# Optimization experiments

Hardware: AMD Instinct MI355X
Metric: run time of the kernel (lower is better)

Reference implementation:

```python
import jax, jax.numpy as jnp
import numpy as np

B, S, H = 32, 128, 768
MH, MT = 6, 8            # max holder / target span sizes
M = max(MH, MT)          # max span size -> M conv widths (1..M)
KH, KT = 4, 4            # max n holders / targets per sentence


def _forward(embedding, mask, wh, bh, wt, bt, wi, bi, we, be):
    Bz, Sz, Hz = embedding.shape
    # --- multi-scale span averaging (Conv1d with identity box filters == moving mean) ---
    cs = jnp.concatenate([jnp.zeros((Bz, 1, Hz), embedding.dtype),
                          jnp.cumsum(embedding, axis=1)], axis=1)  # [B,S+1,H]
    reps = [embedding]
    for w in range(2, M + 1):
        mean = (cs[:, w:, :] - cs[:, :-w, :]) / float(w)          # [B,S-w+1,H]
        reps.append(jnp.pad(mean, ((0, 0), (0, w - 1), (0, 0))))  # zero-pad tail like torch.cat
    span = jnp.concatenate(reps, axis=1)                          # [B, M*S, H]; index = S*width_idx + start
    # --- span validity masks (span must fit within sentence length) ---
    lengths = jnp.sum(mask, axis=1)                               # [B]
    pos = jnp.arange(Sz)
    widths = jnp.arange(M)
    base = pos[None, None, :] < (lengths[:, None, None] - widths[None, :, None])  # [B,M,S]
    holder_valid = (base & (widths[None, :, None] < MH)).reshape(Bz, M * Sz)
    target_valid = (base & (widths[None, :, None] < MT)).reshape(Bz, M * Sz)
    # --- span scoring (sigmoid linear), invalid spans forced to -1 ---
    hs = jnp.where(holder_valid, jax.nn.sigmoid(span @ wh + bh), -1.0)  # [B, M*S]
    ts = jnp.where(target_valid, jax.nn.sigmoid(span @ wt + bt), -1.0)
    # --- top-k span selection (== argsort descending, take first K) ---
    vt, it = jax.lax.top_k(ts, KT)
    vh, ih = jax.lax.top_k(hs, KH)
    tval = vt > 0.0                                                # [B,KT]
    hval = vh > 0.0                                                # [B,KH]
    trep = jnp.take_along_axis(span, it[:, :, None], axis=1)      # [B,KT,H]
    hrep = jnp.take_along_axis(span, ih[:, :, None], axis=1)      # [B,KH,H]
    implicit_input = trep * tval[:, :, None].astype(span.dtype)   # zeros where invalid
    pair_valid = (hval[:, :, None] & tval[:, None, :])            # [B,KH,KT]
    pair = jnp.concatenate([jnp.broadcast_to(hrep[:, :, None, :], (Bz, KH, KT, Hz)),
                            jnp.broadcast_to(trep[:, None, :, :], (Bz, KH, KT, Hz))], axis=-1)
    explicit_input = (pair * pair_valid[..., None].astype(span.dtype)).reshape(Bz, KH * KT, 2 * Hz)
    implicit_logits = implicit_input @ wi + bi                    # [B,KT,4]
    explicit_logits = explicit_input @ we + be                    # [B,KH*KT,4]
    return implicit_logits, explicit_logits, hs, ts


def setup_inputs() -> dict:
    key = jax.random.key(0)
    ks = jax.random.split(key, 8)
    embedding = jax.random.normal(ks[0], (B, S, H), jnp.float32)
    mask = jax.random.randint(ks[1], (B, S), 0, 2).astype(jnp.int32)
    wh = jax.random.normal(ks[2], (H,), jnp.float32) * 0.02
    bh = jnp.zeros((), jnp.float32)
    wt = jax.random.normal(ks[3], (H,), jnp.float32) * 0.02
    bt = jnp.zeros((), jnp.float32)
    wi = jax.random.normal(ks[4], (H, 4), jnp.float32) * 0.02
    bi = jnp.zeros((4,), jnp.float32)
    we = jax.random.normal(ks[5], (2 * H, 4), jnp.float32) * 0.02
    be = jnp.zeros((4,), jnp.float32)
    return dict(embedding=embedding, mask=mask, wh=wh, bh=bh, wt=wt, bt=bt,
                wi=wi, bi=bi, we=we, be=be)


def reference(embedding, mask, wh, bh, wt, bt, wi, bi, we, be):
    return _forward(embedding, mask, wh, bh, wt, bt, wi, bi, we, be)
```

## Files before the change

### kernel.cpp

```cpp
#include <hip/hip_runtime.h>

namespace {
constexpr int Bsz = 32;
constexpr int Ssz = 128;
constexpr int Hsz = 768;
constexpr int Msz = 8;
constexpr int MHs = 6;
constexpr int NSPAN = Msz * Ssz;
}

__device__ __forceinline__ bool gtpair(float av, int ai, float bv, int bi) {
    return (av > bv) || (av == bv && ai < bi);
}

struct Top4 { float v[4]; int ix[4]; };

__device__ __forceinline__ void t4_init(Top4& t) {
#pragma unroll
    for (int k = 0; k < 4; ++k) { t.v[k] = -3.f; t.ix[k] = 0x7fffffff; }
}

__device__ __forceinline__ void t4_insert_g(Top4& a, float cv, int ci) {
    bool g0 = gtpair(cv, ci, a.v[0], a.ix[0]);
    bool g1 = gtpair(cv, ci, a.v[1], a.ix[1]);
    bool g2 = gtpair(cv, ci, a.v[2], a.ix[2]);
    bool g3 = gtpair(cv, ci, a.v[3], a.ix[3]);
    float nv3 = g2 ? a.v[2]  : (g3 ? cv : a.v[3]);
    int   ni3 = g2 ? a.ix[2] : (g3 ? ci : a.ix[3]);
    float nv2 = g1 ? a.v[1]  : (g2 ? cv : a.v[2]);
    int   ni2 = g1 ? a.ix[1] : (g2 ? ci : a.ix[2]);
    float nv1 = g0 ? a.v[0]  : (g1 ? cv : a.v[1]);
    int   ni1 = g0 ? a.ix[0] : (g1 ? ci : a.ix[1]);
    float nv0 = g0 ? cv : a.v[0];
    int   ni0 = g0 ? ci : a.ix[0];
    a.v[0] = nv0; a.ix[0] = ni0;
    a.v[1] = nv1; a.ix[1] = ni1;
    a.v[2] = nv2; a.ix[2] = ni2;
    a.v[3] = nv3; a.ix[3] = ni3;
}

__device__ __forceinline__ void t4_merge_into(Top4& a, const Top4& b) {
#pragma unroll
    for (int k = 0; k < 4; ++k) t4_insert_g(a, b.v[k], b.ix[k]);
}

__device__ __forceinline__ Top4 t4_wave_merge(Top4 t) {
#pragma unroll
    for (int off = 1; off < 64; off <<= 1) {
        Top4 o;
#pragma unroll
        for (int k = 0; k < 4; ++k) {
            o.v[k]  = __shfl_xor(t.v[k], off);
            o.ix[k] = __shfl_xor(t.ix[k], off);
        }
        t4_merge_into(t, o);
    }
    return t;
}

__global__ __launch_bounds__(256) void row_dots_kernel(
    const float* __restrict__ emb, const float* __restrict__ wh,
    const float* __restrict__ wt, float* __restrict__ dh, float* __restrict__ dt)
{
    int row  = blockIdx.x * 4 + (threadIdx.x >> 6);
    int lane = threadIdx.x & 63;
    const float4* r  = (const float4*)(emb + (size_t)row * Hsz);
    const float4* h4 = (const float4*)wh;
    const float4* t4 = (const float4*)wt;
    float ph = 0.f, pt = 0.f;
#pragma unroll
    for (int i = 0; i < 3; ++i) {
        float4 e = r[lane + 64 * i];
        float4 a = h4[lane + 64 * i];
        float4 c = t4[lane + 64 * i];
        ph = fmaf(e.x, a.x, fmaf(e.y, a.y, fmaf(e.z, a.z, fmaf(e.w, a.w, ph))));
        pt = fmaf(e.x, c.x, fmaf(e.y, c.y, fmaf(e.z, c.z, fmaf(e.w, c.w, pt))));
    }
#pragma unroll
    for (int off = 32; off; off >>= 1) {
        ph += __shfl_down(ph, off);
        pt += __shfl_down(pt, off);
    }
    if (lane == 0) { dh[row] = ph; dt[row] = pt; }
}

__global__ __launch_bounds__(256) void per_batch_kernel(
    const float* __restrict__ emb, const int* __restrict__ mask,
    const float* __restrict__ bh_p, const float* __restrict__ bt_p,
    const float* __restrict__ wi, const float* __restrict__ bi,
    const float* __restrict__ we, const float* __restrict__ be,
    const float* __restrict__ dh, const float* __restrict__ dt,
    float* __restrict__ out)
{
    const int b = blockIdx.x;
    const int tid = threadIdx.x;
    const int wavei = tid >> 6, lane = tid & 63;

    __shared__ float dsh[Ssz], dst_[Ssz];
    __shared__ int   len_s;
    __shared__ float swv[4][4];
    __shared__ int   swi[4][4];
    __shared__ int   sel[8];
    __shared__ int   val[8];
    __shared__ float proj[8][8];

    if (tid < Ssz) {
        dsh[tid]  = dh[b * Ssz + tid];
        dst_[tid] = dt[b * Ssz + tid];
    }
    if (wavei == 0) {
        int m = mask[b * Ssz + lane] + mask[b * Ssz + lane + 64];
#pragma unroll
        for (int off = 32; off; off >>= 1) m += __shfl_down(m, off);
        if (lane == 0) len_s = m;
    }
    __syncthreads();

    const int   len = len_s;
    const float bhv = bh_p[0], btv = bt_p[0];
    float* out_impl = out;
    float* out_expl = out + Bsz * 16;
    float* out_hs   = out_expl + Bsz * 64;
    float* out_ts   = out_hs + Bsz * NSPAN;

    {
        const int st  = tid & (Ssz - 1);
        const int grp = tid >> 7;
        const float* dar = grp ? dsh : dst_;
        const float  bv  = grp ? bhv : btv;
        float* outp = grp ? (out_hs + b * NSPAN) : (out_ts + b * NSPAN);
        Top4 t4l; t4_init(t4l);
        float run = 0.f;
#pragma unroll
        for (int widx = 0; widx < Msz; ++widx) {
            bool fits = (st < len - widx);
            if (fits) run += dar[st + widx];
            bool valid = fits && (grp == 0 || widx < MHs);
            float sc = -1.f;
            if (valid) {
                float x = run * (1.f / (float)(widx + 1)) + bv;
                sc = 1.f / (1.f + __expf(-x));
            }
            int i = (widx << 7) | st;
            outp[i] = sc;
            t4_insert_g(t4l, sc, i);
        }
        t4l = t4_wave_merge(t4l);
        if (lane == 0) {
#pragma unroll
            for (int k = 0; k < 4; ++k) { swv[wavei][k] = t4l.v[k]; swi[wavei][k] = t4l.ix[k]; }
        }
    }
    __syncthreads();

    if (tid < 2) {
        Top4 a, c;
#pragma unroll
        for (int k = 0; k < 4; ++k) {
            a.v[k] = swv[2 * tid][k];     a.ix[k] = swi[2 * tid][k];
            c.v[k] = swv[2 * tid + 1][k]; c.ix[k] = swi[2 * tid + 1][k];
        }
        t4_merge_into(a, c);
#pragma unroll
        for (int k = 0; k < 4; ++k) {
            sel[tid * 4 + k] = a.ix[k];
            val[tid * 4 + k] = (a.v[k] > 0.f) ? 1 : 0;
        }
    }
    __syncthreads();

    for (int s2 = 0; s2 < 2; ++s2) {
        int slot = wavei + 4 * s2;
        float acc[8] = {0.f, 0.f, 0.f, 0.f, 0.f, 0.f, 0.f, 0.f};
        if (val[slot]) {
            int idx = sel[slot];
            int w = (idx >> 7) + 1, st = idx & (Ssz - 1);
            const float4* base = (const float4*)(emb + ((size_t)b * Ssz + st) * Hsz);
            float inv = 1.f / (float)w;
            float4 s0 = {0,0,0,0}, s1 = {0,0,0,0}, s2v = {0,0,0,0};
#pragma unroll
            for (int r = 0; r < Msz; ++r) {
                int   rr = (r < w) ? r : (w - 1);
                float m_ = (r < w) ? inv : 0.f;
                const float4* rp = base + rr * (Hsz / 4);
                float4 e0 = rp[lane];
                float4 e1 = rp[lane + 64];
                float4 e2 = rp[lane + 128];
                s0.x = fmaf(e0.x, m_, s0.x); s0.y = fmaf(e0.y, m_, s0.y);
                s0.z = fmaf(e0.z, m_, s0.z); s0.w = fmaf(e0.w, m_, s0.w);
                s1.x = fmaf(e1.x, m_, s1.x); s1.y = fmaf(e1.y, m_, s1.y);
                s1.z = fmaf(e1.z, m_, s1.z); s1.w = fmaf(e1.w, m_, s1.w);
                s2v.x = fmaf(e2.x, m_, s2v.x); s2v.y = fmaf(e2.y, m_, s2v.y);
                s2v.z = fmaf(e2.z, m_, s2v.z); s2v.w = fmaf(e2.w, m_, s2v.w);
            }
            const float4* wi4 = (const float4*)wi;
            const float4* we4 = (const float4*)we;
#pragma unroll
            for (int ii = 0; ii < 3; ++ii) {
                float4 rep = (ii == 0) ? s0 : ((ii == 1) ? s1 : s2v);
                float reps[4] = {rep.x, rep.y, rep.z, rep.w};
                int j = lane + 64 * ii;
                if (s2 == 0) {
#pragma unroll
                    for (int t = 0; t < 4; ++t) {
                        float rt = reps[t];
                        float4 a = wi4[4 * j + t];
                        float4 c = we4[Hsz + 4 * j + t];
                        acc[0] = fmaf(rt, a.x, acc[0]); acc[1] = fmaf(rt, a.y, acc[1]);
                        acc[2] = fmaf(rt, a.z, acc[2]); acc[3] = fmaf(rt, a.w, acc[3]);
                        acc[4] = fmaf(rt, c.x, acc[4]); acc[5] = fmaf(rt, c.y, acc[5]);
                        acc[6] = fmaf(rt, c.z, acc[6]); acc[7] = fmaf(rt, c.w, acc[7]);
                    }
                } else {
#pragma unroll
                    for (int t = 0; t < 4; ++t) {
                        float rt = reps[t];
                        float4 c = we4[4 * j + t];
                        acc[0] = fmaf(rt, c.x, acc[0]); acc[1] = fmaf(rt, c.y, acc[1]);
                        acc[2] = fmaf(rt, c.z, acc[2]); acc[3] = fmaf(rt, c.w, acc[3]);
                    }
                }
            }
        }
#pragma unroll
        for (int off = 32; off; off >>= 1)
#pragma unroll
            for (int c = 0; c < 8; ++c) acc[c] += __shfl_down(acc[c], off);
        if (lane == 0)
#pragma unroll
            for (int c = 0; c < 8; ++c) proj[slot][c] = acc[c];
    }
    __syncthreads();

    if (tid < 16) {
        int k = tid >> 2, c = tid & 3;
        out_impl[b * 16 + tid] = bi[c] + (val[k] ? proj[k][c] : 0.f);
    } else if (tid >= 64 && tid < 128) {
        int u = tid - 64;
        int j = u >> 4, k = (u >> 2) & 3, c = u & 3;
        float v = be[c];
        if (val[4 + j] && val[k]) v += proj[4 + j][c] + proj[k][4 + c];
        out_expl[b * 64 + u] = v;
    }
}

extern "C" void kernel_launch(void* const* d_in, const int* in_sizes, int n_in,
                              void* d_out, int out_size, void* d_ws, size_t ws_size,
                              hipStream_t stream) {
    const float* emb  = (const float*)d_in[0];
    const int*   mask = (const int*)d_in[1];
    const float* wh   = (const float*)d_in[2];
    const float* bh   = (const float*)d_in[3];
    const float* wt   = (const float*)d_in[4];
    const float* bt   = (const float*)d_in[5];
    const float* wi   = (const float*)d_in[6];
    const float* bi   = (const float*)d_in[7];
    const float* we   = (const float*)d_in[8];
    const float* be   = (const float*)d_in[9];
    float* out = (float*)d_out;

    float* dh = (float*)d_ws;
    float* dt = dh + Bsz * Ssz;

    row_dots_kernel<<<(Bsz * Ssz) / 4, 256, 0, stream>>>(emb, wh, wt, dh, dt);
    per_batch_kernel<<<Bsz, 256, 0, stream>>>(emb, mask, bh, bt, wi, bi, we, be,
                                              dh, dt, out);
}
```

Before: 93.87 us.

## Fuse row-dot kernel into per-batch kernel to drop a launch and workspace round trip

Removes the separate row_dots_kernel and computes the holder/target dot products inside the per-batch kernel. Each of the 32 blocks streams its batch's 128 rows with 4 waves, keeping wh/wt in registers, and writes the dots straight to shared memory. This drops a kernel launch and the global workspace write/read. The cost is parallelism: the 12.6 MB embedding read now runs on only 32 blocks instead of 1024, which may leave memory bandwidth underused on a GPU with many CUs.

```diff
diff --git a/kernel.cpp b/kernel.cpp
--- a/kernel.cpp
+++ b/kernel.cpp
@@ -58,38 +58,12 @@
     return t;
 }
 
-__global__ __launch_bounds__(256) void row_dots_kernel(
-    const float* __restrict__ emb, const float* __restrict__ wh,
-    const float* __restrict__ wt, float* __restrict__ dh, float* __restrict__ dt)
-{
-    int row  = blockIdx.x * 4 + (threadIdx.x >> 6);
-    int lane = threadIdx.x & 63;
-    const float4* r  = (const float4*)(emb + (size_t)row * Hsz);
-    const float4* h4 = (const float4*)wh;
-    const float4* t4 = (const float4*)wt;
-    float ph = 0.f, pt = 0.f;
-#pragma unroll
-    for (int i = 0; i < 3; ++i) {
-        float4 e = r[lane + 64 * i];
-        float4 a = h4[lane + 64 * i];
-        float4 c = t4[lane + 64 * i];
-        ph = fmaf(e.x, a.x, fmaf(e.y, a.y, fmaf(e.z, a.z, fmaf(e.w, a.w, ph))));
-        pt = fmaf(e.x, c.x, fmaf(e.y, c.y, fmaf(e.z, c.z, fmaf(e.w, c.w, pt))));
-    }
-#pragma unroll
-    for (int off = 32; off; off >>= 1) {
-        ph += __shfl_down(ph, off);
-        pt += __shfl_down(pt, off);
-    }
-    if (lane == 0) { dh[row] = ph; dt[row] = pt; }
-}
-
-__global__ __launch_bounds__(256) void per_batch_kernel(
+__global__ __launch_bounds__(256) void per_batch_fused(
     const float* __restrict__ emb, const int* __restrict__ mask,
-    const float* __restrict__ bh_p, const float* __restrict__ bt_p,
+    const float* __restrict__ wh, const float* __restrict__ bh_p,
+    const float* __restrict__ wt, const float* __restrict__ bt_p,
     const float* __restrict__ wi, const float* __restrict__ bi,
     const float* __restrict__ we, const float* __restrict__ be,
-    const float* __restrict__ dh, const float* __restrict__ dt,
     float* __restrict__ out)
 {
     const int b = blockIdx.x;
@@ -104,15 +78,39 @@
     __shared__ int   val[8];
     __shared__ float proj[8][8];
 
-    if (tid < Ssz) {
-        dsh[tid]  = dh[b * Ssz + tid];
-        dst_[tid] = dt[b * Ssz + tid];
+    int mcnt = 0;
+    if (wavei == 0)
+        mcnt = mask[b * Ssz + lane] + mask[b * Ssz + lane + 64];
+
+    const float4* wh4 = (const float4*)wh;
+    const float4* wt4 = (const float4*)wt;
+    float4 WH0 = wh4[lane], WH1 = wh4[lane + 64], WH2 = wh4[lane + 128];
+    float4 WT0 = wt4[lane], WT1 = wt4[lane + 64], WT2 = wt4[lane + 128];
+
+    const float4* eb = (const float4*)(emb + (size_t)b * Ssz * Hsz);
+#pragma unroll 4
+    for (int r8 = 0; r8 < 32; ++r8) {
+        int row = wavei * 32 + r8;
+        const float4* rp = eb + row * (Hsz / 4);
+        float4 e0 = rp[lane], e1 = rp[lane + 64], e2 = rp[lane + 128];
+        float ph = 0.f, pt = 0.f;
+        ph = fmaf(e0.x, WH0.x, fmaf(e0.y, WH0.y, fmaf(e0.z, WH0.z, fmaf(e0.w, WH0.w, ph))));
+        ph = fmaf(e1.x, WH1.x, fmaf(e1.y, WH1.y, fmaf(e1.z, WH1.z, fmaf(e1.w, WH1.w, ph))));
+        ph = fmaf(e2.x, WH2.x, fmaf(e2.y, WH2.y, fmaf(e2.z, WH2.z, fmaf(e2.w, WH2.w, ph))));
+        pt = fmaf(e0.x, WT0.x, fmaf(e0.y, WT0.y, fmaf(e0.z, WT0.z, fmaf(e0.w, WT0.w, pt))));
+        pt = fmaf(e1.x, WT1.x, fmaf(e1.y, WT1.y, fmaf(e1.z, WT1.z, fmaf(e1.w, WT1.w, pt))));
+        pt = fmaf(e2.x, WT2.x, fmaf(e2.y, WT2.y, fmaf(e2.z, WT2.z, fmaf(e2.w, WT2.w, pt))));
+#pragma unroll
+        for (int off = 32; off; off >>= 1) {
+            ph += __shfl_down(ph, off);
+            pt += __shfl_down(pt, off);
+        }
+        if (lane == 0) { dsh[row] = ph; dst_[row] = pt; }
     }
     if (wavei == 0) {
-        int m = mask[b * Ssz + lane] + mask[b * Ssz + lane + 64];
-#pragma unroll
-        for (int off = 32; off; off >>= 1) m += __shfl_down(m, off);
-        if (lane == 0) len_s = m;
+#pragma unroll
+        for (int off = 32; off; off >>= 1) mcnt += __shfl_down(mcnt, off);
+        if (lane == 0) len_s = mcnt;
     }
     __syncthreads();
 
@@ -175,7 +173,7 @@
         if (val[slot]) {
             int idx = sel[slot];
             int w = (idx >> 7) + 1, st = idx & (Ssz - 1);
-            const float4* base = (const float4*)(emb + ((size_t)b * Ssz + st) * Hsz);
+            const float4* base = eb + (size_t)st * (Hsz / 4);
             float inv = 1.f / (float)w;
             float4 s0 = {0,0,0,0}, s1 = {0,0,0,0}, s2v = {0,0,0,0};
 #pragma unroll
@@ -259,10 +257,6 @@
     const float* be   = (const float*)d_in[9];
     float* out = (float*)d_out;
 
-    float* dh = (float*)d_ws;
-    float* dt = dh + Bsz * Ssz;
-
-    row_dots_kernel<<<(Bsz * Ssz) / 4, 256, 0, stream>>>(emb, wh, wt, dh, dt);
-    per_batch_kernel<<<Bsz, 256, 0, stream>>>(emb, mask, bh, bt, wi, bi, we, be,
-                                              dh, dt, out);
-}
+    per_batch_fused<<<Bsz, 256, 0, stream>>>(emb, mask, wh, bh, wt, bt,
+                                             wi, bi, we, be, out);
+}
```

Result: slower. 108.1 us (+15.2%).
